# Performance work log

Measured on AMD Instinct MI355X. Metric: run time of the kernel, lower is better.

Reference implementation:

```python
import jax, jax.numpy as jnp
import numpy as np

N_NODES = 50000
N_EDGES = 800000
N_REL = 8
DIM = 256


def setup_inputs() -> dict:
    key = jax.random.key(0)
    ks = jax.random.split(key, 6)
    x = jax.random.normal(ks[0], (N_NODES, DIM), dtype=jnp.float32)
    # xavier-uniform-ish scale for [R, in, out] weights
    limit = float(np.sqrt(6.0 / (DIM + DIM)))
    W0 = jax.random.uniform(ks[1], (N_REL, DIM, DIM), dtype=jnp.float32, minval=-limit, maxval=limit)
    W1 = jax.random.uniform(ks[2], (N_REL, DIM, DIM), dtype=jnp.float32, minval=-limit, maxval=limit)
    b0 = jnp.zeros((DIM,), dtype=jnp.float32)
    b1 = jnp.zeros((DIM,), dtype=jnp.float32)
    edge_index = jax.random.randint(ks[3], (2, N_EDGES), 0, N_NODES, dtype=jnp.int64)
    edge_type = jax.random.randint(ks[4], (N_EDGES,), 0, N_REL, dtype=jnp.int64)
    return {"x": x, "W0": W0, "b0": b0, "W1": W1, "b1": b1,
            "edge_index": edge_index, "edge_type": edge_type}


def _rgcn_layer(x, W, b, src, dst, edge_type, num_nodes):
    # grouped GEMM over all relations: [R, N, out]
    xt = jnp.einsum('ni,rio->rno', x, W)
    # per-edge message = relu(x[src] @ W[edge_type] + b)  -> [E, out]
    msg = jax.nn.relu(xt[edge_type, src] + b)
    # scatter-add into destination nodes
    return jax.ops.segment_sum(msg, dst, num_segments=num_nodes)


def reference(x, W0, b0, W1, b1, edge_index, edge_type):
    src, dst = edge_index[0], edge_index[1]
    h = _rgcn_layer(x, W0, b0, src, dst, edge_type, x.shape[0])
    h = _rgcn_layer(h, W1, b1, src, dst, edge_type, x.shape[0])
    return h
```

## Files before the change

### kernel.cpp

```cpp
#include <hip/hip_runtime.h>

#define DIM 256
#define N_REL 8

typedef __attribute__((ext_vector_type(8))) short short8_t;
typedef __attribute__((ext_vector_type(4))) float float4_t;

__device__ inline unsigned short f2bf(float f) {
    unsigned u = __float_as_uint(f);
    u += 0x7FFFu + ((u >> 16) & 1u);
    return (unsigned short)(u >> 16);
}
__device__ inline float bf2f(unsigned short h) {
    return __uint_as_float(((unsigned)h) << 16);
}

__global__ __launch_bounds__(256) void prep_mega(
    const float* __restrict__ x, unsigned short* __restrict__ xb, int n4,
    const float* __restrict__ W0, unsigned short* __restrict__ Wt0,
    const float* __restrict__ W1, unsigned short* __restrict__ Wt1,
    const int* __restrict__ dst, int E, int* __restrict__ cnt,
    int nCast, int nW)
{
    __shared__ float tile[32][33];
    const int b = blockIdx.x;
    const int t = threadIdx.x;
    if (b < nCast) {
        const int i = b * 256 + t;
        if (i < n4) {
            const float4 v = ((const float4*)x)[i];
            ushort4 o;
            o.x = f2bf(v.x); o.y = f2bf(v.y); o.z = f2bf(v.z); o.w = f2bf(v.w);
            ((ushort4*)xb)[i] = o;
        }
    } else if (b < nCast + 2 * nW) {
        const int wi = b - nCast;
        const float* W = (wi < nW) ? W0 : W1;
        unsigned short* Wt = (wi < nW) ? Wt0 : Wt1;
        const int bb = (wi < nW) ? wi : wi - nW;
        const int rel = bb >> 6;
        const int bx = bb & 7, by = (bb >> 3) & 7;
        const int i0 = bx * 32, o0 = by * 32;
        const int tx = t & 31, ty = t >> 5;
        const float* Wr = W + (size_t)rel * DIM * DIM;
        unsigned short* Wtr = Wt + (size_t)rel * DIM * DIM;
#pragma unroll
        for (int j = 0; j < 4; j++)
            tile[ty + 8 * j][tx] = Wr[(size_t)(i0 + ty + 8 * j) * DIM + o0 + tx];
        __syncthreads();
#pragma unroll
        for (int j = 0; j < 4; j++)
            Wtr[(size_t)(o0 + ty + 8 * j) * DIM + i0 + tx] =
                f2bf(tile[tx][ty + 8 * j]);
    } else {
        const int e = (b - nCast - 2 * nW) * 256 + t;
        if (e < E) atomicAdd(&cnt[dst[e]], 1);
    }
}

__global__ __launch_bounds__(256) void gemm_mfma_bias_relu(
    const unsigned short* __restrict__ Xb,
    const unsigned short* __restrict__ Wtb,
    const float* __restrict__ bias,
    unsigned short* __restrict__ Yall, int M, int Rtiles)
{
    __shared__ __align__(16) short smem[16384];

    const unsigned L = blockIdx.x;
    const int xcd = L & 7;
    const unsigned g = L >> 3;
    const int combo = g & 15;
    const int rt = (int)((g >> 4) << 3) | xcd;
    if (rt >= Rtiles) return;
    const int m0 = rt * 128;
    const int n0 = (combo & 1) * 128;
    const int rel = combo >> 1;

    const unsigned short* Wt = Wtb + (size_t)rel * DIM * DIM;
    unsigned short* Y = Yall + (size_t)rel * M * DIM;

    const int t = threadIdx.x;
    const int lane = t & 63;
    const int w = t >> 6;
    const int wr = w & 1, wc = w >> 1;
    const int r = lane & 15, q = lane >> 4;

    const int sl = lane & 3;
    const int rsub = lane >> 2;
    const unsigned short* gA[2];
    const unsigned short* gB[2];
#pragma unroll
    for (int h = 0; h < 2; h++) {
        const int row = h * 64 + w * 16 + rsub;
        const int gseg = sl ^ ((row >> 1) & 3);
        gA[h] = Xb + (size_t)(m0 + row) * DIM + gseg * 8;
        gB[h] = Wt + (size_t)(n0 + row) * DIM + gseg * 8;
    }

    const int swz = (q ^ ((r >> 1) & 3)) * 8;
    int offA[4], offB[4];
#pragma unroll
    for (int mi = 0; mi < 4; mi++)
        offA[mi] = (wr * 64 + mi * 16 + r) * 32 + swz;
#pragma unroll
    for (int ni = 0; ni < 4; ni++)
        offB[ni] = (wc * 64 + ni * 16 + r) * 32 + swz;

    float4_t acc[4][4];
#pragma unroll
    for (int i = 0; i < 4; i++)
#pragma unroll
        for (int j = 0; j < 4; j++) {
            float4_t z = {0.f, 0.f, 0.f, 0.f};
            acc[i][j] = z;
        }

#define STAGE(ks, bsel)                                                         \
    {                                                                           \
        const int k0_ = (ks) * 32;                                              \
        short* Ad_ = smem + ((bsel) ? 8192 : 0);                                \
        short* Bd_ = Ad_ + 4096;                                                \
        _Pragma("unroll")                                                       \
        for (int h = 0; h < 2; h++) {                                           \
            __builtin_amdgcn_global_load_lds(                                   \
                (const __attribute__((address_space(1))) unsigned int*)(gA[h] + k0_), \
                (__attribute__((address_space(3))) unsigned int*)(Ad_ + h * 2048 + w * 512), \
                16, 0, 0);                                                      \
            __builtin_amdgcn_global_load_lds(                                   \
                (const __attribute__((address_space(1))) unsigned int*)(gB[h] + k0_), \
                (__attribute__((address_space(3))) unsigned int*)(Bd_ + h * 2048 + w * 512), \
                16, 0, 0);                                                      \
        }                                                                       \
    }

    STAGE(0, 0);
#pragma unroll 1
    for (int ks = 0; ks < 8; ks++) {
        const int cur = ks & 1;
        if (ks < 7) {
            STAGE(ks + 1, cur ^ 1);
            asm volatile("s_waitcnt vmcnt(4)" ::: "memory");
        } else {
            asm volatile("s_waitcnt vmcnt(0)" ::: "memory");
        }
        asm volatile("s_barrier" ::: "memory");

        const short* As_b = smem + (cur ? 8192 : 0);
        const short* Bs_b = As_b + 4096;
        short8_t af[4], bf[4];
#pragma unroll
        for (int mi = 0; mi < 4; mi++)
            af[mi] = *(const short8_t*)&As_b[offA[mi]];
#pragma unroll
        for (int ni = 0; ni < 4; ni++)
            bf[ni] = *(const short8_t*)&Bs_b[offB[ni]];
#pragma unroll
        for (int mi = 0; mi < 4; mi++)
#pragma unroll
            for (int ni = 0; ni < 4; ni++)
                acc[mi][ni] = __builtin_amdgcn_mfma_f32_16x16x32_bf16(
                    af[mi], bf[ni], acc[mi][ni], 0, 0, 0);
        asm volatile("s_barrier" ::: "memory");
    }
#undef STAGE

    short* St = smem;

    float bv[4];
#pragma unroll
    for (int ni = 0; ni < 4; ni++)
        bv[ni] = bias[n0 + wc * 64 + ni * 16 + r];

#pragma unroll
    for (int mp = 0; mp < 2; mp++) {
#pragma unroll
        for (int s = 0; s < 2; s++) {
#pragma unroll
            for (int ni = 0; ni < 4; ni++) {
#pragma unroll
                for (int e = 0; e < 4; e++) {
                    const int rl = s * 32 + wr * 16 + q * 4 + e;
                    const int col = wc * 64 + ni * 16 + r;
                    St[rl * 136 + col] =
                        f2bf(fmaxf(acc[mp * 2 + s][ni][e] + bv[ni], 0.f));
                }
            }
        }
        __syncthreads();
#pragma unroll
        for (int j = 0; j < 4; j++) {
            const int id = t + 256 * j;
            const int rl2 = id >> 4;
            const int ch = id & 15;
            const int s = rl2 >> 5;
            const int rl = rl2 & 31;
            const int grow = m0 + (rl >> 4) * 64 + (mp * 2 + s) * 16 + (rl & 15);
            const short8_t v = *(const short8_t*)&St[rl2 * 136 + ch * 8];
            if (grow < M)
                *(short8_t*)&Y[(size_t)grow * DIM + n0 + ch * 8] = v;
        }
        if (mp == 0) __syncthreads();
    }
}

__global__ __launch_bounds__(256) void scan_blocksums(
    const int* __restrict__ cnt, int N, int* __restrict__ bsum)
{
    __shared__ int red[256];
    const int t = threadIdx.x;
    const int base = blockIdx.x * 1024 + t * 4;
    int s = 0;
#pragma unroll
    for (int j = 0; j < 4; j++) {
        const int i = base + j;
        if (i < N) s += cnt[i];
    }
    red[t] = s;
    __syncthreads();
#pragma unroll
    for (int off = 128; off > 0; off >>= 1) {
        if (t < off) red[t] += red[t + off];
        __syncthreads();
    }
    if (t == 0) bsum[blockIdx.x] = red[0];
}

__global__ __launch_bounds__(256) void scan_write(
    const int* __restrict__ cnt, int N, const int* __restrict__ bsum, int nb,
    int* __restrict__ rowptr, int* __restrict__ cursor)
{
    __shared__ int sb[64];
    __shared__ int sh[256];
    const int t = threadIdx.x;
    if (t < 64) sb[t] = (t < nb) ? bsum[t] : 0;
    __syncthreads();
    for (int off = 1; off < 64; off <<= 1) {
        int v = 0;
        if (t < 64) v = sb[t] + ((t >= off) ? sb[t - off] : 0);
        __syncthreads();
        if (t < 64) sb[t] = v;
        __syncthreads();
    }
    const int run0 = (blockIdx.x == 0) ? 0 : sb[blockIdx.x - 1];
    const int total = sb[nb - 1];

    const int base = blockIdx.x * 1024 + t * 4;
    int v[4];
#pragma unroll
    for (int j = 0; j < 4; j++) {
        const int i = base + j;
        v[j] = (i < N) ? cnt[i] : 0;
    }
    sh[t] = v[0] + v[1] + v[2] + v[3];
    __syncthreads();
    for (int off = 1; off < 256; off <<= 1) {
        const int add = (t >= off) ? sh[t - off] : 0;
        __syncthreads();
        sh[t] += add;
        __syncthreads();
    }
    int run = run0 + ((t == 0) ? 0 : sh[t - 1]);
#pragma unroll
    for (int j = 0; j < 4; j++) {
        const int i = base + j;
        if (i < N) { rowptr[i] = run; cursor[i] = run; }
        run += v[j];
    }
    if ((int)blockIdx.x == nb - 1 && t == 255) rowptr[N] = total;
}

__global__ __launch_bounds__(256) void fill_edges(
    const int* __restrict__ src, const int* __restrict__ dst,
    const int* __restrict__ et, int E, int* __restrict__ cursor,
    unsigned* __restrict__ ep)
{
    const int e = blockIdx.x * blockDim.x + threadIdx.x;
    if (e >= E) return;
    const int pos = atomicAdd(&cursor[dst[e]], 1);
    ep[pos] = (unsigned)src[e] | ((unsigned)et[e] << 16);
}

template <typename OT>
__global__ __launch_bounds__(256) void aggregate2x(
    const unsigned short* __restrict__ yall,
    const unsigned* __restrict__ ep, const int* __restrict__ rowptr,
    OT* __restrict__ out, int M)
{
    const int lane = threadIdx.x & 63;
    const int half = lane >> 5;
    const int cl = lane & 31;
    const int wv = (blockIdx.x * blockDim.x + threadIdx.x) >> 6;
    const int nw = (gridDim.x * blockDim.x) >> 6;
    const size_t plane = (size_t)M * DIM;
    const int npair = (M + 1) >> 1;

    for (int pr = wv; pr < npair; pr += nw) {
        const int d = 2 * pr + half;
        const bool live = (d < M);
        double acc[8];
#pragma unroll
        for (int j = 0; j < 8; j++) acc[j] = 0.0;

        int beg = 0, end = 0;
        if (live) { beg = rowptr[d]; end = rowptr[d + 1]; }

        for (int c0 = beg; c0 < end; c0 += 32) {
            const int n = min(32, end - c0);
            const unsigned myep = (c0 + cl < end) ? ep[c0 + cl] : 0u;
            for (int i = 0; i < n; i += 4) {
                short8_t u[4];
#pragma unroll
                for (int j = 0; j < 4; j++) {
                    const unsigned p = __shfl(myep, half * 32 + ((i + j) & 31));
                    u[j] = *(const short8_t*)(
                        yall + (size_t)(p >> 16) * plane +
                        (size_t)(p & 0xFFFFu) * DIM + cl * 8);
                }
#pragma unroll
                for (int j = 0; j < 4; j++) {
                    if (i + j < n) {
#pragma unroll
                        for (int k = 0; k < 8; k++)
                            acc[k] += (double)bf2f((unsigned short)u[j][k]);
                    }
                }
            }
        }
        if (live) {
            OT* dp = out + (size_t)d * DIM + cl * 8;
            if (sizeof(OT) == 4) {
                *(float4*)((float*)dp) = make_float4(
                    (float)acc[0], (float)acc[1], (float)acc[2], (float)acc[3]);
                *(float4*)((float*)dp + 4) = make_float4(
                    (float)acc[4], (float)acc[5], (float)acc[6], (float)acc[7]);
            } else {
                short8_t v;
#pragma unroll
                for (int j = 0; j < 8; j++) v[j] = (short)f2bf((float)acc[j]);
                *(short8_t*)((unsigned short*)dp) = v;
            }
        }
    }
}

__global__ __launch_bounds__(256) void gemm_bias_relu_f32(
    const float* __restrict__ A, const float* __restrict__ B,
    const float* __restrict__ bias, float* __restrict__ Y, int M)
{
    __shared__ float Asf[16][132];
    __shared__ float Bsf[16][128];
    const int t = threadIdx.x;
    const int tx = t & 15, ty = t >> 4;
    const int row0 = blockIdx.x * 128, col0 = blockIdx.y * 128;
    float acc[8][8];
#pragma unroll
    for (int i = 0; i < 8; i++)
#pragma unroll
        for (int j = 0; j < 8; j++) acc[i][j] = 0.f;
    const int arow = t >> 2, akseg = (t & 3) * 4;
    const int bk0 = t >> 5, bcol = (t & 31) * 4;
    for (int k0 = 0; k0 < DIM; k0 += 16) {
#pragma unroll
        for (int h = 0; h < 2; h++) {
            const int row = row0 + arow + h * 64;
            float4 av = (row < M) ? *(const float4*)(A + (size_t)row * DIM + k0 + akseg)
                                  : make_float4(0, 0, 0, 0);
            Asf[akseg + 0][arow + h * 64] = av.x;
            Asf[akseg + 1][arow + h * 64] = av.y;
            Asf[akseg + 2][arow + h * 64] = av.z;
            Asf[akseg + 3][arow + h * 64] = av.w;
        }
#pragma unroll
        for (int h = 0; h < 2; h++) {
            const int krow = bk0 + h * 8;
            *(float4*)&Bsf[krow][bcol] =
                *(const float4*)(B + (size_t)(k0 + krow) * DIM + col0 + bcol);
        }
        __syncthreads();
#pragma unroll
        for (int k = 0; k < 16; k++) {
            float a[8], b[8];
            *(float4*)&a[0] = *(const float4*)&Asf[k][ty * 4];
            *(float4*)&a[4] = *(const float4*)&Asf[k][64 + ty * 4];
            *(float4*)&b[0] = *(const float4*)&Bsf[k][tx * 4];
            *(float4*)&b[4] = *(const float4*)&Bsf[k][64 + tx * 4];
#pragma unroll
            for (int i = 0; i < 8; i++)
#pragma unroll
                for (int j = 0; j < 8; j++) acc[i][j] = fmaf(a[i], b[j], acc[i][j]);
        }
        __syncthreads();
    }
#pragma unroll
    for (int im = 0; im < 2; im++)
#pragma unroll
        for (int i = 0; i < 4; i++) {
            const int row = row0 + im * 64 + ty * 4 + i;
            if (row >= M) continue;
#pragma unroll
            for (int jm = 0; jm < 2; jm++) {
                const int col = col0 + jm * 64 + tx * 4;
                const float4 bb = *(const float4*)(bias + col);
                float4 o;
                o.x = fmaxf(acc[im * 4 + i][jm * 4 + 0] + bb.x, 0.f);
                o.y = fmaxf(acc[im * 4 + i][jm * 4 + 1] + bb.y, 0.f);
                o.z = fmaxf(acc[im * 4 + i][jm * 4 + 2] + bb.z, 0.f);
                o.w = fmaxf(acc[im * 4 + i][jm * 4 + 3] + bb.w, 0.f);
                *(float4*)(Y + (size_t)row * DIM + col) = o;
            }
        }
}

__global__ __launch_bounds__(256) void scatter_rel(
    const float* __restrict__ y, const int* __restrict__ src,
    const int* __restrict__ dst, const int* __restrict__ et,
    int rel, float* __restrict__ out, int n_edges)
{
    const int lane = threadIdx.x & 63;
    const int wave = (blockIdx.x * blockDim.x + threadIdx.x) >> 6;
    const int nwaves = (gridDim.x * blockDim.x) >> 6;
    for (int e = wave; e < n_edges; e += nwaves) {
        if (et[e] != rel) continue;
        const float4 v = *(const float4*)(y + (size_t)src[e] * DIM + lane * 4);
        float* o = out + (size_t)dst[e] * DIM + lane * 4;
        atomicAdd(o + 0, v.x);
        atomicAdd(o + 1, v.y);
        atomicAdd(o + 2, v.z);
        atomicAdd(o + 3, v.w);
    }
}

static inline size_t align16(size_t x) { return (x + 15) & ~(size_t)15; }

extern "C" void kernel_launch(void* const* d_in, const int* in_sizes, int n_in,
                              void* d_out, int out_size, void* d_ws, size_t ws_size,
                              hipStream_t stream)
{
    const float* x  = (const float*)d_in[0];
    const float* W0 = (const float*)d_in[1];
    const float* b0 = (const float*)d_in[2];
    const float* W1 = (const float*)d_in[3];
    const float* b1 = (const float*)d_in[4];
    const int* eidx = (const int*)d_in[5];
    const int* etyp = (const int*)d_in[6];

    const int M = in_sizes[0] / DIM;
    const int E = in_sizes[6];
    const int* src = eidx;
    const int* dst = eidx + E;
    float* out = (float*)d_out;

    const size_t plane = (size_t)M * DIM;
    const size_t wbytes = (size_t)N_REL * DIM * DIM * 2;

    const size_t need = align16(plane * 2)
                      + align16(plane * 2)
                      + 2 * align16(wbytes)
                      + align16((size_t)(M + 1) * 4)
                      + 2 * align16((size_t)M * 4)
                      + align16((size_t)256 * 4)
                      + align16((size_t)E * 4)
                      + align16((size_t)N_REL * plane * 2);

    if (M < 65536 && ws_size >= need) {
        char* ws = (char*)d_ws;
        size_t off = 0;
        unsigned short* h1b  = (unsigned short*)(ws + off); off = align16(off + plane * 2);
        unsigned short* xb   = (unsigned short*)(ws + off); off = align16(off + plane * 2);
        unsigned short* Wt0b = (unsigned short*)(ws + off); off = align16(off + wbytes);
        unsigned short* Wt1b = (unsigned short*)(ws + off); off = align16(off + wbytes);
        int* rowptr = (int*)(ws + off); off = align16(off + (size_t)(M + 1) * 4);
        int* cnt    = (int*)(ws + off); off = align16(off + (size_t)M * 4);
        int* cursor = (int*)(ws + off); off = align16(off + (size_t)M * 4);
        int* bsum   = (int*)(ws + off); off = align16(off + (size_t)256 * 4);
        unsigned* ep = (unsigned*)(ws + off); off = align16(off + (size_t)E * 4);
        unsigned short* yall = (unsigned short*)(ws + off);

        const int n4 = (int)(plane / 4);
        const int nCast = (n4 + 255) / 256;
        const int nW = 512;
        const int nCnt = (E + 255) / 256;
        hipMemsetAsync(cnt, 0, (size_t)M * 4, stream);
        prep_mega<<<nCast + 2 * nW + nCnt, 256, 0, stream>>>(
            x, xb, n4, W0, Wt0b, W1, Wt1b, dst, E, cnt, nCast, nW);

        const int nb = (M + 1023) / 1024;
        scan_blocksums<<<nb, 256, 0, stream>>>(cnt, M, bsum);
        scan_write<<<nb, 256, 0, stream>>>(cnt, M, bsum, nb, rowptr, cursor);
        fill_edges<<<(E + 255) / 256, 256, 0, stream>>>(src, dst, etyp, E, cursor, ep);

        const int Rtiles = (M + 127) / 128;
        const int octets = (Rtiles + 7) / 8;
        const int ggrid = octets * 16 * 8;
        const int npair = (M + 1) / 2;
        const int agrid = (npair * 64 + 255) / 256;

        gemm_mfma_bias_relu<<<ggrid, 256, 0, stream>>>(xb, Wt0b, b0, yall, M, Rtiles);
        aggregate2x<unsigned short><<<agrid, 256, 0, stream>>>(yall, ep, rowptr, h1b, M);
        gemm_mfma_bias_relu<<<ggrid, 256, 0, stream>>>(h1b, Wt1b, b1, yall, M, Rtiles);
        aggregate2x<float><<<agrid, 256, 0, stream>>>(yall, ep, rowptr, out, M);
    } else {
        float* h1 = (float*)d_ws;
        float* y  = (float*)d_ws + plane;
        const dim3 gblk(256), ggrid2((M + 127) / 128, DIM / 128);
        hipMemsetAsync(h1, 0, plane * 4, stream);
        for (int r = 0; r < N_REL; r++) {
            gemm_bias_relu_f32<<<ggrid2, gblk, 0, stream>>>(
                x, W0 + (size_t)r * DIM * DIM, b0, y, M);
            scatter_rel<<<1024, 256, 0, stream>>>(y, src, dst, etyp, r, h1, E);
        }
        hipMemsetAsync(out, 0, plane * 4, stream);
        for (int r = 0; r < N_REL; r++) {
            gemm_bias_relu_f32<<<ggrid2, gblk, 0, stream>>>(
                h1, W1 + (size_t)r * DIM * DIM, b1, y, M);
            scatter_rel<<<1024, 256, 0, stream>>>(y, src, dst, etyp, r, out, E);
        }
    }
}
```

Baseline: 497.4 us.

## Build destination CSR with two-pass shared-memory bucket sort instead of global atomics

Edge CSR construction no longer uses global atomic counting and atomic cursor fills. Edges are packed into 64-bit keys and then placed in two passes. The first pass scatters by high destination byte using per-block histograms and a global scan. The second sorts each bucket by low byte in shared memory and emits per-node counts. The goal is to remove contended random global atomics and scattered writes, at the cost of more kernel launches and extra 64-bit key traffic staged in the yall buffer.

```diff
diff --git a/kernel.cpp b/kernel.cpp
--- a/kernel.cpp
+++ b/kernel.cpp
@@ -2,6 +2,8 @@
 
 #define DIM 256
 #define N_REL 8
+#define NBLK 256
+#define NBH 256
 
 typedef __attribute__((ext_vector_type(8))) short short8_t;
 typedef __attribute__((ext_vector_type(4))) float float4_t;
@@ -19,7 +21,6 @@
     const float* __restrict__ x, unsigned short* __restrict__ xb, int n4,
     const float* __restrict__ W0, unsigned short* __restrict__ Wt0,
     const float* __restrict__ W1, unsigned short* __restrict__ Wt1,
-    const int* __restrict__ dst, int E, int* __restrict__ cnt,
     int nCast, int nW)
 {
     __shared__ float tile[32][33];
@@ -33,7 +34,7 @@
             o.x = f2bf(v.x); o.y = f2bf(v.y); o.z = f2bf(v.z); o.w = f2bf(v.w);
             ((ushort4*)xb)[i] = o;
         }
-    } else if (b < nCast + 2 * nW) {
+    } else {
         const int wi = b - nCast;
         const float* W = (wi < nW) ? W0 : W1;
         unsigned short* Wt = (wi < nW) ? Wt0 : Wt1;
@@ -52,9 +53,150 @@
         for (int j = 0; j < 4; j++)
             Wtr[(size_t)(o0 + ty + 8 * j) * DIM + i0 + tx] =
                 f2bf(tile[tx][ty + 8 * j]);
-    } else {
-        const int e = (b - nCast - 2 * nW) * 256 + t;
-        if (e < E) atomicAdd(&cnt[dst[e]], 1);
+    }
+}
+
+__global__ __launch_bounds__(256) void build_keys_hist(
+    const int* __restrict__ src, const int* __restrict__ dst,
+    const int* __restrict__ et, int E,
+    unsigned long long* __restrict__ e0, int* __restrict__ hist)
+{
+    __shared__ int lh[NBH];
+    const int t = threadIdx.x, b = blockIdx.x;
+    lh[t] = 0;
+    __syncthreads();
+    const int chunk = (E + NBLK - 1) / NBLK;
+    const int lo = b * chunk, hi = min(lo + chunk, E);
+    for (int i = lo + t; i < hi; i += 256) {
+        const unsigned d = (unsigned)dst[i];
+        e0[i] = ((unsigned long long)d << 32) |
+                ((unsigned)((et[i] << 16) | src[i]));
+        atomicAdd(&lh[d >> 8], 1);
+    }
+    __syncthreads();
+    hist[t * NBLK + b] = lh[t];
+}
+
+__global__ __launch_bounds__(256) void scan_g_blocksums(
+    const int* __restrict__ a, int n, int* __restrict__ bsum)
+{
+    __shared__ int red[256];
+    const int t = threadIdx.x;
+    const int base = blockIdx.x * 1024 + t * 4;
+    int s = 0;
+#pragma unroll
+    for (int j = 0; j < 4; j++) {
+        const int i = base + j;
+        if (i < n) s += a[i];
+    }
+    red[t] = s;
+    __syncthreads();
+#pragma unroll
+    for (int off = 128; off > 0; off >>= 1) {
+        if (t < off) red[t] += red[t + off];
+        __syncthreads();
+    }
+    if (t == 0) bsum[blockIdx.x] = red[0];
+}
+
+__global__ __launch_bounds__(256) void scan_g_write(
+    const int* __restrict__ a, int n, const int* __restrict__ bsum, int nb,
+    int* __restrict__ outArr, int* __restrict__ totalSlot)
+{
+    __shared__ int sb[64];
+    __shared__ int sh[256];
+    const int t = threadIdx.x;
+    if (t < 64) sb[t] = (t < nb) ? bsum[t] : 0;
+    __syncthreads();
+    for (int off = 1; off < 64; off <<= 1) {
+        int v = 0;
+        if (t < 64) v = sb[t] + ((t >= off) ? sb[t - off] : 0);
+        __syncthreads();
+        if (t < 64) sb[t] = v;
+        __syncthreads();
+    }
+    const int run0 = (blockIdx.x == 0) ? 0 : sb[blockIdx.x - 1];
+    const int total = sb[nb - 1];
+
+    const int base = blockIdx.x * 1024 + t * 4;
+    int v[4];
+#pragma unroll
+    for (int j = 0; j < 4; j++) {
+        const int i = base + j;
+        v[j] = (i < n) ? a[i] : 0;
+    }
+    sh[t] = v[0] + v[1] + v[2] + v[3];
+    __syncthreads();
+    for (int off = 1; off < 256; off <<= 1) {
+        const int add = (t >= off) ? sh[t - off] : 0;
+        __syncthreads();
+        sh[t] += add;
+        __syncthreads();
+    }
+    int run = run0 + ((t == 0) ? 0 : sh[t - 1]);
+#pragma unroll
+    for (int j = 0; j < 4; j++) {
+        const int i = base + j;
+        if (i < n) outArr[i] = run;
+        run += v[j];
+    }
+    if (totalSlot && (int)blockIdx.x == nb - 1 && t == 255) *totalSlot = total;
+}
+
+__global__ __launch_bounds__(256) void scatter_pass1(
+    const unsigned long long* __restrict__ e0, int E,
+    const int* __restrict__ histx, unsigned long long* __restrict__ e1)
+{
+    __shared__ int lbase[NBH];
+    __shared__ int lrun[NBH];
+    const int t = threadIdx.x, b = blockIdx.x;
+    lbase[t] = histx[t * NBLK + b];
+    lrun[t] = 0;
+    __syncthreads();
+    const int chunk = (E + NBLK - 1) / NBLK;
+    const int lo = b * chunk, hi = min(lo + chunk, E);
+    for (int i = lo + t; i < hi; i += 256) {
+        const unsigned long long v = e0[i];
+        const int bin = (int)(v >> 40) & 0xFF;
+        const int pos = lbase[bin] + atomicAdd(&lrun[bin], 1);
+        e1[pos] = v;
+    }
+}
+
+__global__ __launch_bounds__(256) void bucket_sort(
+    const unsigned long long* __restrict__ e1, int E,
+    const int* __restrict__ histx,
+    unsigned* __restrict__ ep, int* __restrict__ cnt)
+{
+    __shared__ int lh[256], lincl[256], lexcl[256], lrun[256];
+    const int t = threadIdx.x;
+    const int h = blockIdx.x;
+    const int start = histx[h * NBLK];
+    const int end = (h == NBH - 1) ? E : histx[(h + 1) * NBLK];
+    if (end <= start) return;
+    lh[t] = 0;
+    __syncthreads();
+    for (int i = start + t; i < end; i += 256)
+        atomicAdd(&lh[(int)(e1[i] >> 32) & 0xFF], 1);
+    __syncthreads();
+    const int v = lh[t];
+    lincl[t] = v;
+    __syncthreads();
+    for (int off = 1; off < 256; off <<= 1) {
+        const int add = (t >= off) ? lincl[t - off] : 0;
+        __syncthreads();
+        lincl[t] += add;
+        __syncthreads();
+    }
+    lexcl[t] = lincl[t] - v;
+    lrun[t] = 0;
+    if (v > 0) cnt[(h << 8) | t] = v;
+    __syncthreads();
+    for (int i = start + t; i < end; i += 256) {
+        const unsigned long long x = e1[i];
+        const int low = (int)(x >> 32) & 0xFF;
+        const int pos = lexcl[low] + atomicAdd(&lrun[low], 1);
+        ep[start + pos] = (unsigned)(x & 0xFFFFFFFFu);
     }
 }
 
@@ -203,83 +345,6 @@
     }
 }
 
-__global__ __launch_bounds__(256) void scan_blocksums(
-    const int* __restrict__ cnt, int N, int* __restrict__ bsum)
-{
-    __shared__ int red[256];
-    const int t = threadIdx.x;
-    const int base = blockIdx.x * 1024 + t * 4;
-    int s = 0;
-#pragma unroll
-    for (int j = 0; j < 4; j++) {
-        const int i = base + j;
-        if (i < N) s += cnt[i];
-    }
-    red[t] = s;
-    __syncthreads();
-#pragma unroll
-    for (int off = 128; off > 0; off >>= 1) {
-        if (t < off) red[t] += red[t + off];
-        __syncthreads();
-    }
-    if (t == 0) bsum[blockIdx.x] = red[0];
-}
-
-__global__ __launch_bounds__(256) void scan_write(
-    const int* __restrict__ cnt, int N, const int* __restrict__ bsum, int nb,
-    int* __restrict__ rowptr, int* __restrict__ cursor)
-{
-    __shared__ int sb[64];
-    __shared__ int sh[256];
-    const int t = threadIdx.x;
-    if (t < 64) sb[t] = (t < nb) ? bsum[t] : 0;
-    __syncthreads();
-    for (int off = 1; off < 64; off <<= 1) {
-        int v = 0;
-        if (t < 64) v = sb[t] + ((t >= off) ? sb[t - off] : 0);
-        __syncthreads();
-        if (t < 64) sb[t] = v;
-        __syncthreads();
-    }
-    const int run0 = (blockIdx.x == 0) ? 0 : sb[blockIdx.x - 1];
-    const int total = sb[nb - 1];
-
-    const int base = blockIdx.x * 1024 + t * 4;
-    int v[4];
-#pragma unroll
-    for (int j = 0; j < 4; j++) {
-        const int i = base + j;
-        v[j] = (i < N) ? cnt[i] : 0;
-    }
-    sh[t] = v[0] + v[1] + v[2] + v[3];
-    __syncthreads();
-    for (int off = 1; off < 256; off <<= 1) {
-        const int add = (t >= off) ? sh[t - off] : 0;
-        __syncthreads();
-        sh[t] += add;
-        __syncthreads();
-    }
-    int run = run0 + ((t == 0) ? 0 : sh[t - 1]);
-#pragma unroll
-    for (int j = 0; j < 4; j++) {
-        const int i = base + j;
-        if (i < N) { rowptr[i] = run; cursor[i] = run; }
-        run += v[j];
-    }
-    if ((int)blockIdx.x == nb - 1 && t == 255) rowptr[N] = total;
-}
-
-__global__ __launch_bounds__(256) void fill_edges(
-    const int* __restrict__ src, const int* __restrict__ dst,
-    const int* __restrict__ et, int E, int* __restrict__ cursor,
-    unsigned* __restrict__ ep)
-{
-    const int e = blockIdx.x * blockDim.x + threadIdx.x;
-    if (e >= E) return;
-    const int pos = atomicAdd(&cursor[dst[e]], 1);
-    ep[pos] = (unsigned)src[e] | ((unsigned)et[e] << 16);
-}
-
 template <typename OT>
 __global__ __launch_bounds__(256) void aggregate2x(
     const unsigned short* __restrict__ yall,
@@ -452,17 +517,19 @@
 
     const size_t plane = (size_t)M * DIM;
     const size_t wbytes = (size_t)N_REL * DIM * DIM * 2;
+    const size_t yall_bytes = (size_t)N_REL * plane * 2;
 
     const size_t need = align16(plane * 2)
                       + align16(plane * 2)
                       + 2 * align16(wbytes)
                       + align16((size_t)(M + 1) * 4)
-                      + 2 * align16((size_t)M * 4)
+                      + align16((size_t)M * 4)
                       + align16((size_t)256 * 4)
+                      + align16((size_t)NBH * NBLK * 4)
                       + align16((size_t)E * 4)
-                      + align16((size_t)N_REL * plane * 2);
-
-    if (M < 65536 && ws_size >= need) {
+                      + align16(yall_bytes);
+
+    if (M < 65536 && ws_size >= need && yall_bytes >= 2 * (size_t)E * 8) {
         char* ws = (char*)d_ws;
         size_t off = 0;
         unsigned short* h1b  = (unsigned short*)(ws + off); off = align16(off + plane * 2);
@@ -471,23 +538,30 @@
         unsigned short* Wt1b = (unsigned short*)(ws + off); off = align16(off + wbytes);
         int* rowptr = (int*)(ws + off); off = align16(off + (size_t)(M + 1) * 4);
         int* cnt    = (int*)(ws + off); off = align16(off + (size_t)M * 4);
-        int* cursor = (int*)(ws + off); off = align16(off + (size_t)M * 4);
         int* bsum   = (int*)(ws + off); off = align16(off + (size_t)256 * 4);
+        int* hist   = (int*)(ws + off); off = align16(off + (size_t)NBH * NBLK * 4);
         unsigned* ep = (unsigned*)(ws + off); off = align16(off + (size_t)E * 4);
         unsigned short* yall = (unsigned short*)(ws + off);
+        unsigned long long* e64a = (unsigned long long*)yall;
+        unsigned long long* e64b = e64a + E;
 
         const int n4 = (int)(plane / 4);
         const int nCast = (n4 + 255) / 256;
         const int nW = 512;
-        const int nCnt = (E + 255) / 256;
+        prep_mega<<<nCast + 2 * nW, 256, 0, stream>>>(
+            x, xb, n4, W0, Wt0b, W1, Wt1b, nCast, nW);
+
         hipMemsetAsync(cnt, 0, (size_t)M * 4, stream);
-        prep_mega<<<nCast + 2 * nW + nCnt, 256, 0, stream>>>(
-            x, xb, n4, W0, Wt0b, W1, Wt1b, dst, E, cnt, nCast, nW);
-
+        build_keys_hist<<<NBLK, 256, 0, stream>>>(src, dst, etyp, E, e64a, hist);
+        const int nhist = NBH * NBLK;
+        const int nbh = (nhist + 1023) / 1024;
+        scan_g_blocksums<<<nbh, 256, 0, stream>>>(hist, nhist, bsum);
+        scan_g_write<<<nbh, 256, 0, stream>>>(hist, nhist, bsum, nbh, hist, (int*)nullptr);
+        scatter_pass1<<<NBLK, 256, 0, stream>>>(e64a, E, hist, e64b);
+        bucket_sort<<<NBH, 256, 0, stream>>>(e64b, E, hist, ep, cnt);
         const int nb = (M + 1023) / 1024;
-        scan_blocksums<<<nb, 256, 0, stream>>>(cnt, M, bsum);
-        scan_write<<<nb, 256, 0, stream>>>(cnt, M, bsum, nb, rowptr, cursor);
-        fill_edges<<<(E + 255) / 256, 256, 0, stream>>>(src, dst, etyp, E, cursor, ep);
+        scan_g_blocksums<<<nb, 256, 0, stream>>>(cnt, M, bsum);
+        scan_g_write<<<nb, 256, 0, stream>>>(cnt, M, bsum, nb, rowptr, &rowptr[M]);
 
         const int Rtiles = (M + 127) / 128;
         const int octets = (Rtiles + 7) / 8;
```

Measured after the change: 469.3 us. -5.6%, faster.
